# Kernel tuning notes

Hardware: AMD Instinct MI355X
Metric: run time of the kernel (lower is better)

The kernel has to match this reference:

```python
import jax, jax.numpy as jnp
import numpy as np
from jax import lax


def conv2d(x, w, b, pad):
    y = lax.conv_general_dilated(x, w, (1, 1), [(pad, pad), (pad, pad)],
                                 dimension_numbers=('NCHW', 'OIHW', 'NCHW'))
    return y + b[None, :, None, None]


def grid_sample_bilinear_border(img, grid):
    # img [B,C,H,W], grid [B,h,w,2] normalized to [-1,1] (x,y), align_corners=False
    B, C, H, W = img.shape
    gx, gy = grid[..., 0], grid[..., 1]
    ix = jnp.clip(((gx + 1.0) * W - 1.0) * 0.5, 0.0, W - 1.0)  # border padding = clamp coords
    iy = jnp.clip(((gy + 1.0) * H - 1.0) * 0.5, 0.0, H - 1.0)
    x0f, y0f = jnp.floor(ix), jnp.floor(iy)
    wx, wy = ix - x0f, iy - y0f                       # [B,h,w]
    x0 = jnp.clip(x0f.astype(jnp.int32), 0, W - 1)
    y0 = jnp.clip(y0f.astype(jnp.int32), 0, H - 1)
    x1 = jnp.clip(x0 + 1, 0, W - 1)
    y1 = jnp.clip(y0 + 1, 0, H - 1)
    gather = jax.vmap(lambda im, yi, xi: im[:, yi, xi])  # -> [B,C,h,w]
    v00 = gather(img, y0, x0)
    v01 = gather(img, y0, x1)
    v10 = gather(img, y1, x0)
    v11 = gather(img, y1, x1)
    wx, wy = wx[:, None], wy[:, None]                  # [B,1,h,w]
    return (v00 * (1 - wx) * (1 - wy) + v01 * wx * (1 - wy)
            + v10 * (1 - wx) * wy + v11 * wx * wy)


def setup_inputs():
    key = jax.random.key(0)
    ks = jax.random.split(key, 16)
    B, Ch, H, W = 8, 256, 64, 64
    Cl, h, w = 128, 128, 128
    Co, r = 128, 8
    s = 0.05
    return {
        'f_high': jax.random.normal(ks[0], (B, Ch, H, W), jnp.float32),
        'f_low': jax.random.normal(ks[1], (B, Cl, h, w), jnp.float32),
        'off_w1': jax.random.normal(ks[2], (64, Ch + Cl, 3, 3), jnp.float32) * s,
        'off_b1': jnp.zeros((64,), jnp.float32),
        'off_w2': jax.random.normal(ks[3], (2, 64, 3, 3), jnp.float32) * s,
        'off_b2': jnp.zeros((2,), jnp.float32),
        'proj_w': jax.random.normal(ks[4], (Co, Ch), jnp.float32) * s,
        'proj_b': jnp.zeros((Co,), jnp.float32),
        'ca_w1': jax.random.normal(ks[5], (Co // r, Co), jnp.float32) * s,
        'ca_b1': jnp.zeros((Co // r,), jnp.float32),
        'ca_w2': jax.random.normal(ks[6], (Co, Co // r), jnp.float32) * s,
        'ca_b2': jnp.zeros((Co,), jnp.float32),
        'sa_w': jax.random.normal(ks[7], (1, 2, 7, 7), jnp.float32) * s,
        'sa_b': jnp.zeros((1,), jnp.float32),
    }


def reference(f_high, f_low, off_w1, off_b1, off_w2, off_b2,
              proj_w, proj_b, ca_w1, ca_b1, ca_w2, ca_b2, sa_w, sa_b):
    B, Ch, H, W = f_high.shape
    _, Cl, h, w = f_low.shape
    # resize f_high to (h,w) (bilinear, half-pixel centers == align_corners=False)
    fh_r = jax.image.resize(f_high, (B, Ch, h, w), 'bilinear', antialias=False)
    cat = jnp.concatenate([fh_r, f_low], axis=1)       # [B,Ch+Cl,h,w]
    hid = jax.nn.relu(conv2d(cat, off_w1, off_b1, 1))
    offset = conv2d(hid, off_w2, off_b2, 1)            # [B,2,h,w]
    # base normalized grid (x,y) in [-1,1]
    ys = jnp.linspace(-1.0, 1.0, h, dtype=f_high.dtype)
    xs = jnp.linspace(-1.0, 1.0, w, dtype=f_high.dtype)
    gy, gx = jnp.meshgrid(ys, xs, indexing='ij')
    base = jnp.stack([gx, gy], axis=-1)[None]          # [1,h,w,2]
    scale = jnp.array([2.0 / w, 2.0 / h], dtype=f_high.dtype)
    grid = base + offset.transpose(0, 2, 3, 1) * scale  # [B,h,w,2]
    f_aligned = grid_sample_bilinear_border(f_high, grid)  # [B,Ch,h,w]
    # 1x1 proj Ch -> Co
    x = jnp.einsum('oc,bchw->bohw', proj_w, f_aligned) + proj_b[None, :, None, None]
    # multi-attention fusion: channel (SE) then spatial (CBAM-style)
    p = x.mean(axis=(2, 3))                            # [B,Co]
    a = jax.nn.sigmoid(jax.nn.relu(p @ ca_w1.T + ca_b1) @ ca_w2.T + ca_b2)
    xc = x * a[:, :, None, None]
    sm = jnp.concatenate([xc.mean(axis=1, keepdims=True),
                          xc.max(axis=1, keepdims=True)], axis=1)  # [B,2,h,w]
    sa = jax.nn.sigmoid(conv2d(sm, sa_w, sa_b, 3))
    return xc * sa
```

## Files before the change

kernel.cpp:

```cpp
#include <hip/hip_runtime.h>
#include <hip/hip_fp16.h>
#include <math.h>

typedef _Float16 f16;
typedef _Float16 f16x8 __attribute__((ext_vector_type(8)));
typedef _Float16 f16x2 __attribute__((ext_vector_type(2)));
typedef float f32x4 __attribute__((ext_vector_type(4)));

__device__ __forceinline__ void gll16(const void* g, void* l) {
  __builtin_amdgcn_global_load_lds((const __attribute__((address_space(1))) void*)g,
                                   (__attribute__((address_space(3))) void*)l, 16, 0, 0);
}

__global__ __launch_bounds__(256) void pack_conv_w(const float* __restrict__ w,
                                                   f16* __restrict__ out,
                                                   int CIN, int MFR, int COUT) {
  int idx = blockIdx.x * 256 + threadIdx.x;
  int KC = CIN / 32;
  int total = 9 * KC * MFR * 64 * 8;
  if (idx >= total) return;
  int j = idx & 7;
  int lane = (idx >> 3) & 63;
  int rest = idx >> 9;
  int mf = rest % MFR; rest /= MFR;
  int kc = rest % KC; int t = rest / KC;
  int oc = mf * 16 + (lane & 15);
  int c = kc * 32 + (lane >> 4) * 8 + j;
  int ky = t / 3, kx = t % 3;
  float v = (oc < COUT) ? w[((oc * CIN + c) * 3 + ky) * 3 + kx] : 0.f;
  out[idx] = (f16)v;
}

__global__ __launch_bounds__(256) void pack_proj_w(const float* __restrict__ w,
                                                   f16* __restrict__ out) {
  int idx = blockIdx.x * 256 + threadIdx.x;
  int j = idx & 7; int lane = (idx >> 3) & 63; int rest = idx >> 9;
  int mf = rest & 7; int kc = rest >> 3;
  int oc = mf * 16 + (lane & 15);
  int c = kc * 32 + (lane >> 4) * 8 + j;
  out[idx] = (f16)w[oc * 256 + c];
}

__global__ __launch_bounds__(256) void k_zero(f16* __restrict__ cat, f16* __restrict__ hid) {
  int idx = blockIdx.x * 256 + threadIdx.x;
  f16x8 z = {(f16)0, (f16)0, (f16)0, (f16)0, (f16)0, (f16)0, (f16)0, (f16)0};
  int p, b, c8;
  f16* dst; int C;
  if (idx < 198144) {
    c8 = idx % 48; int rest = idx / 48; p = rest % 516; b = rest / 516;
    dst = cat; C = 384;
  } else {
    int i2 = idx - 198144;
    c8 = i2 % 8; int rest = i2 / 8; p = rest % 516; b = rest / 516;
    dst = hid; C = 64;
  }
  int y, x;
  if (p < 130) { y = 0; x = p; }
  else if (p < 260) { y = 129; x = p - 130; }
  else if (p < 388) { y = p - 260 + 1; x = 0; }
  else { y = p - 388 + 1; x = 129; }
  *(f16x8*)&dst[(((size_t)b * 130 + y) * 130 + x) * C + c8 * 8] = z;
}

__global__ __launch_bounds__(256) void k_fhw(const float* __restrict__ fh,
                                             f16* __restrict__ fhw) {
  __shared__ float lds[128 * 17];
  int wg = blockIdx.x;
  int xt = wg & 3; int ch2 = (wg >> 2) & 1; int y = (wg >> 3) & 63; int b = wg >> 9;
  int x0 = xt * 16;
  int tid = threadIdx.x;
  for (int i = 0; i < 8; ++i) {
    int u = i * 256 + tid;
    int c = u >> 4, xi = u & 15;
    lds[c * 17 + xi] = fh[(((size_t)b * 256 + ch2 * 128 + c) * 64 + y) * 64 + x0 + xi];
  }
  __syncthreads();
  {
    int x = tid >> 4, cl = tid & 15;
    f16x8 v;
    #pragma unroll
    for (int j = 0; j < 8; ++j) v[j] = (f16)lds[(cl * 8 + j) * 17 + x];
    int coct = ch2 * 16 + cl;
    *(f16x8*)&fhw[(((size_t)b * 64 + y) * 64 + x0 + x) * 256 + coct * 8] = v;
  }
}

__global__ __launch_bounds__(256) void k_catA(const f16* __restrict__ fhw,
                                              f16* __restrict__ cat) {
  int wg = blockIdx.x;
  int Y = wg & 127, b = wg >> 7;
  float iy = fminf(fmaxf(Y * 0.5f - 0.25f, 0.f), 63.f);
  int y0 = (int)iy; float wy = iy - y0; int y1 = min(y0 + 1, 63);
  int tid = threadIdx.x;
  for (int i = 0; i < 16; ++i) {
    int u = i * 256 + tid; int X = u >> 5, coct = u & 31;
    float ix = fminf(fmaxf(X * 0.5f - 0.25f, 0.f), 63.f);
    int x0 = (int)ix; float wx = ix - x0; int x1 = min(x0 + 1, 63);
    f16x8 v00 = *(const f16x8*)&fhw[(((size_t)b * 64 + y0) * 64 + x0) * 256 + coct * 8];
    f16x8 v01 = *(const f16x8*)&fhw[(((size_t)b * 64 + y0) * 64 + x1) * 256 + coct * 8];
    f16x8 v10 = *(const f16x8*)&fhw[(((size_t)b * 64 + y1) * 64 + x0) * 256 + coct * 8];
    f16x8 v11 = *(const f16x8*)&fhw[(((size_t)b * 64 + y1) * 64 + x1) * 256 + coct * 8];
    f16x8 r;
    #pragma unroll
    for (int j = 0; j < 8; ++j) {
      float t0 = (1.f - wx) * (float)v00[j] + wx * (float)v01[j];
      float t1 = (1.f - wx) * (float)v10[j] + wx * (float)v11[j];
      r[j] = (f16)((1.f - wy) * t0 + wy * t1);
    }
    *(f16x8*)&cat[(((size_t)b * 130 + 1 + Y) * 130 + 1 + X) * 384 + coct * 8] = r;
  }
}

__global__ __launch_bounds__(256) void k_catB(const float* __restrict__ fl,
                                              f16* __restrict__ cat) {
  __shared__ float lds[128 * 17];
  int wg = blockIdx.x;
  int xt = wg & 7; int Y = (wg >> 3) & 127; int b = wg >> 10;
  int x0 = xt * 16; int tid = threadIdx.x;
  for (int i = 0; i < 8; ++i) {
    int u = i * 256 + tid; int c = u >> 4, xi = u & 15;
    lds[c * 17 + xi] = fl[(((size_t)b * 128 + c) * 128 + Y) * 128 + x0 + xi];
  }
  __syncthreads();
  {
    int x = tid >> 4, coct = tid & 15;
    f16x8 v;
    #pragma unroll
    for (int j = 0; j < 8; ++j) v[j] = (f16)lds[(coct * 8 + j) * 17 + x];
    *(f16x8*)&cat[(((size_t)b * 130 + 1 + Y) * 130 + 1 + x0 + x) * 384 + 256 + coct * 8] = v;
  }
}

template<int CIN, int MFR, int COUT, bool RELU, int OPAD, int NR, bool FORCE1>
__global__ __launch_bounds__(256, FORCE1 ? 1 : 2) void k_conv3(const f16* __restrict__ in,
                                                               const f16* __restrict__ apack,
                                                               const float* __restrict__ bias,
                                                               f16* __restrict__ out) {
  constexpr int KC = CIN / 32;
  constexpr int TROWS = 4 * NR;
  constexpr int TY = 128 / TROWS;
  constexpr int NSLOT = (TROWS + 2) * 18 * 4;
  constexpr int NPAD = (NSLOT + 255) & ~255;
  constexpr int ROUNDS = NPAD / 256;
  constexpr int PATCH = NPAD * 16;
  constexpr int EPI = TROWS * 16 * COUT * 2;
  constexpr int LDS_SZ = (2 * PATCH > EPI ? 2 * PATCH : EPI) + (FORCE1 ? 1024 : 0);
  __shared__ __align__(16) char ldsb[LDS_SZ];
  int wg = blockIdx.x;
  int b = wg & 7; int t = wg >> 3;
  int ty = t % TY, tx = t / TY;
  int y0 = ty * TROWS, x0 = tx * 16;
  int tid = threadIdx.x, lane = tid & 63, w = tid >> 6;
  int lx = lane & 15, hi = lane >> 4;
  int wN = w * NR;

  int ro[ROUNDS];
  #pragma unroll
  for (int j = 0; j < ROUNDS; ++j) {
    int s = j * 256 + w * 64 + lane;
    if (s > NSLOT - 1) s = NSLOT - 1;
    int p = s >> 2, coct = s & 3;
    int py = p / 18, px = p % 18;
    int cocts = coct ^ ((px >> 1) & 3);
    ro[j] = ((y0 + py) * 130 + (x0 + px)) * CIN + cocts * 8;
  }
  const f16* inb = in + (size_t)b * 130 * 130 * CIN;

  f32x4 acc[MFR][NR];
  #pragma unroll
  for (int m = 0; m < MFR; ++m)
    #pragma unroll
    for (int n = 0; n < NR; ++n) acc[m][n] = (f32x4){0.f, 0.f, 0.f, 0.f};

  auto stage = [&](int kc, int buf) {
    #pragma unroll
    for (int j = 0; j < ROUNDS; ++j)
      gll16(inb + ro[j] + kc * 32, ldsb + buf * PATCH + (j * 256 + w * 64) * 16);
  };

  stage(0, 0);
  __syncthreads();
  for (int kc = 0; kc < KC; ++kc) {
    if (kc + 1 < KC) stage(kc + 1, (kc + 1) & 1);
    const char* cb = ldsb + (kc & 1) * PATCH;
    __builtin_amdgcn_s_setprio(1);
    #pragma unroll
    for (int kx = 0; kx < 3; ++kx) {
      int px = lx + kx;
      int sw = (px >> 1) & 3;
      f16x8 bf[NR + 2];
      #pragma unroll
      for (int s = 0; s < NR + 2; ++s) {
        int slot = ((wN + s) * 18 + px) * 4 + (hi ^ sw);
        bf[s] = *(const f16x8*)(cb + slot * 16);
      }
      #pragma unroll
      for (int ky = 0; ky < 3; ++ky) {
        f16x8 af[MFR];
        #pragma unroll
        for (int m = 0; m < MFR; ++m)
          af[m] = *(const f16x8*)&apack[(size_t)((((ky * 3 + kx) * KC + kc) * MFR + m) * 64 + lane) * 8];
        #pragma unroll
        for (int n = 0; n < NR; ++n)
          #pragma unroll
          for (int m = 0; m < MFR; ++m)
            acc[m][n] = __builtin_amdgcn_mfma_f32_16x16x32_f16(af[m], bf[n + ky], acc[m][n], 0, 0, 0);
      }
    }
    __builtin_amdgcn_s_setprio(0);
    __syncthreads();
  }

  constexpr int S = 128 + 2 * OPAD;
  #pragma unroll
  for (int m = 0; m < MFR; ++m)
    #pragma unroll
    for (int n = 0; n < NR; ++n) {
      int pos = (wN + n) * 16 + lx;
      #pragma unroll
      for (int rp = 0; rp < 2; ++rp) {
        int ch = m * 16 + hi * 4 + rp * 2;
        if (ch < COUT) {
          float v0 = acc[m][n][rp * 2 + 0] + bias[ch];
          float v1 = acc[m][n][rp * 2 + 1] + bias[ch + 1];
          if (RELU) { v0 = fmaxf(v0, 0.f); v1 = fmaxf(v1, 0.f); }
          f16x2 pk; pk[0] = (f16)v0; pk[1] = (f16)v1;
          int addr = ((pos * COUT + ch) * 2) ^ ((pos & 7) << 4);
          *(f16x2*)(ldsb + addr) = pk;
        }
      }
    }
  __syncthreads();
  if constexpr (COUT % 8 == 0) {
    for (int u = tid; u < TROWS * 16 * COUT / 8; u += 256) {
      int pos = u / (COUT / 8); int cp = u % (COUT / 8);
      int addr = ((pos * COUT + cp * 8) * 2) ^ ((pos & 7) << 4);
      f16x8 v = *(const f16x8*)(ldsb + addr);
      int y = y0 + (pos >> 4) + OPAD, x = x0 + (pos & 15) + OPAD;
      *(f16x8*)&out[(((size_t)b * S + y) * S + x) * COUT + cp * 8] = v;
    }
  } else {
    for (int u = tid; u < TROWS * 16 * COUT / 2; u += 256) {
      int pos = u / (COUT / 2); int cp = u % (COUT / 2);
      int addr = ((pos * COUT + cp * 2) * 2) ^ ((pos & 7) << 4);
      f16x2 v = *(const f16x2*)(ldsb + addr);
      int y = y0 + (pos >> 4) + OPAD, x = x0 + (pos & 15) + OPAD;
      *(f16x2*)&out[(((size_t)b * S + y) * S + x) * COUT + cp * 2] = v;
    }
  }
}

__global__ __launch_bounds__(256) void k_gp(const f16* __restrict__ fhw,
                                            const f16* __restrict__ off,
                                            const f16* __restrict__ ppack,
                                            const float* __restrict__ pbias,
                                            f16* __restrict__ x,
                                            float* __restrict__ psum) {
  __shared__ f16 bt[64 * 256];
  __shared__ float4 samp[64];
  char* ldsb = (char*)bt;
  int wg = blockIdx.x;
  int b = wg & 7, tile = wg >> 3;
  int pbase = tile * 64;
  int tid = threadIdx.x, lane = tid & 63, w = tid >> 6;
  if (tid < 64) {
    int pos = pbase + tid;
    int yy = pos >> 7, xx = pos & 127;
    float o0 = (float)off[((size_t)b * 16384 + pos) * 2 + 0];
    float o1 = (float)off[((size_t)b * 16384 + pos) * 2 + 1];
    float gx = -1.f + xx * (2.f / 127.f) + o0 * (1.f / 64.f);
    float gy = -1.f + yy * (2.f / 127.f) + o1 * (1.f / 64.f);
    float ix = fminf(fmaxf((gx + 1.f) * 32.f - 0.5f, 0.f), 63.f);
    float iy = fminf(fmaxf((gy + 1.f) * 32.f - 0.5f, 0.f), 63.f);
    float x0f = floorf(ix), y0f = floorf(iy);
    samp[tid] = make_float4(x0f, y0f, ix - x0f, iy - y0f);
  }
  __syncthreads();
  for (int i = 0; i < 8; ++i) {
    int u = i * 256 + tid; int p = u >> 5, coct = u & 31;
    float4 s = samp[p];
    int x0i = (int)s.x, y0i = (int)s.y;
    int x1i = min(x0i + 1, 63), y1i = min(y0i + 1, 63);
    float wx = s.z, wy = s.w;
    const f16* bb = fhw + (size_t)b * 4096 * 256 + coct * 8;
    f16x8 v00 = *(const f16x8*)&bb[(y0i * 64 + x0i) * 256];
    f16x8 v01 = *(const f16x8*)&bb[(y0i * 64 + x1i) * 256];
    f16x8 v10 = *(const f16x8*)&bb[(y1i * 64 + x0i) * 256];
    f16x8 v11 = *(const f16x8*)&bb[(y1i * 64 + x1i) * 256];
    f16x8 r;
    #pragma unroll
    for (int j = 0; j < 8; ++j) {
      float t0 = (1.f - wx) * (float)v00[j] + wx * (float)v01[j];
      float t1 = (1.f - wx) * (float)v10[j] + wx * (float)v11[j];
      r[j] = (f16)((1.f - wy) * t0 + wy * t1);
    }
    int addr = (p * 512 + coct * 16) ^ ((p & 7) << 4);
    *(f16x8*)(ldsb + addr) = r;
  }
  __syncthreads();
  f32x4 acc[2][4];
  #pragma unroll
  for (int m = 0; m < 2; ++m)
    #pragma unroll
    for (int n = 0; n < 4; ++n) acc[m][n] = (f32x4){0.f, 0.f, 0.f, 0.f};
  #pragma unroll
  for (int kc = 0; kc < 8; ++kc) {
    f16x8 af[2];
    #pragma unroll
    for (int m = 0; m < 2; ++m)
      af[m] = *(const f16x8*)&ppack[(size_t)((kc * 8 + w * 2 + m) * 64 + lane) * 8];
    #pragma unroll
    for (int n = 0; n < 4; ++n) {
      int p = n * 16 + (lane & 15);
      int addr = (p * 512 + kc * 64 + ((lane >> 4) * 16)) ^ ((p & 7) << 4);
      f16x8 bf = *(const f16x8*)(ldsb + addr);
      #pragma unroll
      for (int m = 0; m < 2; ++m)
        acc[m][n] = __builtin_amdgcn_mfma_f32_16x16x32_f16(af[m], bf, acc[m][n], 0, 0, 0);
    }
  }
  __syncthreads();
  #pragma unroll
  for (int m = 0; m < 2; ++m)
    #pragma unroll
    for (int n = 0; n < 4; ++n) {
      int p = n * 16 + (lane & 15);
      #pragma unroll
      for (int r = 0; r < 4; ++r) {
        int ch = w * 32 + m * 16 + (lane >> 4) * 4 + r;
        int addr = ((p * 128 + ch) * 4) ^ ((p & 7) << 4);
        *(float*)(ldsb + addr) = acc[m][n][r];
      }
    }
  __syncthreads();
  float part0 = 0.f, part1 = 0.f;
  int cp = tid & 63, wv = tid >> 6;
  int c0 = cp * 2;
  float b0 = pbias[c0], b1 = pbias[c0 + 1];
  #pragma unroll
  for (int i = 0; i < 16; ++i) {
    int p = i * 4 + wv;
    float v0 = *(const float*)(ldsb + (((p * 128 + c0) * 4) ^ ((p & 7) << 4)));
    float v1 = *(const float*)(ldsb + (((p * 128 + c0 + 1) * 4) ^ ((p & 7) << 4)));
    v0 += b0; v1 += b1;
    f16x2 pk; pk[0] = (f16)v0; pk[1] = (f16)v1;
    *(f16x2*)&x[((size_t)b * 16384 + pbase + p) * 128 + c0] = pk;
    part0 += v0; part1 += v1;
  }
  __syncthreads();
  float* rl = (float*)ldsb;
  rl[wv * 128 + c0] = part0; rl[wv * 128 + c0 + 1] = part1;
  __syncthreads();
  if (tid < 128)
    psum[(size_t)wg * 128 + tid] = rl[tid] + rl[128 + tid] + rl[256 + tid] + rl[384 + tid];
}

__global__ __launch_bounds__(128) void k_ca(const float* __restrict__ psum,
                                            const float* __restrict__ w1, const float* __restrict__ b1,
                                            const float* __restrict__ w2, const float* __restrict__ b2,
                                            float* __restrict__ a) {
  __shared__ float pl[128];
  __shared__ float hl[16];
  int b = blockIdx.x; int tid = threadIdx.x;
  float s = 0.f;
  for (int t = 0; t < 256; ++t) s += psum[(size_t)(t * 8 + b) * 128 + tid];
  pl[tid] = s * (1.f / 16384.f);
  __syncthreads();
  if (tid < 16) {
    float h = b1[tid];
    for (int c = 0; c < 128; ++c) h += pl[c] * w1[tid * 128 + c];
    hl[tid] = fmaxf(h, 0.f);
  }
  __syncthreads();
  float z = b2[tid];
  #pragma unroll
  for (int o2 = 0; o2 < 16; ++o2) z += hl[o2] * w2[tid * 16 + o2];
  a[b * 128 + tid] = 1.f / (1.f + expf(-z));
}

__global__ __launch_bounds__(256) void k_sm(const f16* __restrict__ x,
                                            const float* __restrict__ a,
                                            float* __restrict__ meanp, float* __restrict__ maxp) {
  __shared__ float al[128];
  int wg = blockIdx.x;
  int pbase = wg * 128;
  int b = pbase >> 14;
  int tid = threadIdx.x;
  if (tid < 128) al[tid] = a[b * 128 + tid];
  __syncthreads();
  #pragma unroll
  for (int i = 0; i < 8; ++i) {
    int u = i * 256 + tid;
    int p = u >> 4, q = u & 15;
    f16x8 v = *(const f16x8*)&x[((size_t)pbase + p) * 128 + q * 8];
    float sm = 0.f, mx = -1e30f;
    #pragma unroll
    for (int j = 0; j < 8; ++j) {
      float xc = (float)v[j] * al[q * 8 + j];
      sm += xc; mx = fmaxf(mx, xc);
    }
    #pragma unroll
    for (int d = 1; d < 16; d <<= 1) {
      sm += __shfl_xor(sm, d);
      mx = fmaxf(mx, __shfl_xor(mx, d));
    }
    if ((tid & 15) == 0) {
      meanp[pbase + p] = sm * (1.f / 128.f);
      maxp[pbase + p] = mx;
    }
  }
}

__global__ __launch_bounds__(256) void k_sa(const float* __restrict__ meanp,
                                            const float* __restrict__ maxp,
                                            const float* __restrict__ sw, const float* __restrict__ sb,
                                            float* __restrict__ sap) {
  __shared__ float lds[2][22][22];
  __shared__ float wl[98];
  int wg = blockIdx.x;
  int tx = wg & 7, ty = (wg >> 3) & 7, b = wg >> 6;
  int y0 = ty * 16, x0 = tx * 16;
  int tid = threadIdx.x;
  if (tid < 98) wl[tid] = sw[tid];
  for (int u = tid; u < 2 * 22 * 22; u += 256) {
    int ch = u / 484; int p = u % 484; int py = p / 22, px = p % 22;
    int gy = y0 + py - 3, gx = x0 + px - 3;
    float v = 0.f;
    if (gy >= 0 && gy < 128 && gx >= 0 && gx < 128)
      v = ch ? maxp[(size_t)b * 16384 + gy * 128 + gx] : meanp[(size_t)b * 16384 + gy * 128 + gx];
    lds[ch][py][px] = v;
  }
  __syncthreads();
  int py = tid >> 4, px = tid & 15;
  float accv = sb[0];
  #pragma unroll
  for (int ch = 0; ch < 2; ++ch)
    for (int ky = 0; ky < 7; ++ky)
      #pragma unroll
      for (int kx = 0; kx < 7; ++kx)
        accv += lds[ch][py + ky][px + kx] * wl[ch * 49 + ky * 7 + kx];
  sap[(size_t)b * 16384 + (y0 + py) * 128 + x0 + px] = 1.f / (1.f + expf(-accv));
}

__global__ __launch_bounds__(256) void k_out(const f16* __restrict__ x,
                                             const float* __restrict__ a,
                                             const float* __restrict__ sap,
                                             float* __restrict__ out) {
  __shared__ float lds[32 * 129];
  __shared__ float al[128];
  __shared__ float sl[32];
  int wg = blockIdx.x;
  int pbase = wg * 32; int b = pbase >> 14;
  int tid = threadIdx.x;
  if (tid < 128) al[tid] = a[b * 128 + tid];
  if (tid < 32) sl[tid] = sap[pbase + tid];
  __syncthreads();
  #pragma unroll
  for (int i = 0; i < 2; ++i) {
    int u = i * 256 + tid;
    int p = u >> 4, q = u & 15;
    f16x8 v = *(const f16x8*)&x[((size_t)pbase + p) * 128 + q * 8];
    #pragma unroll
    for (int j = 0; j < 8; ++j) lds[p * 129 + q * 8 + j] = (float)v[j];
  }
  __syncthreads();
  #pragma unroll
  for (int i = 0; i < 16; ++i) {
    int u = i * 256 + tid; int c = u >> 5, p = u & 31;
    float v = lds[p * 129 + c] * al[c] * sl[p];
    out[((size_t)(b * 128 + c)) * 16384 + (pbase & 16383) + p] = v;
  }
}

extern "C" void kernel_launch(void* const* d_in, const int* in_sizes, int n_in,
                              void* d_out, int out_size, void* d_ws, size_t ws_size,
                              hipStream_t stream) {
  const float* f_high = (const float*)d_in[0];
  const float* f_low  = (const float*)d_in[1];
  const float* off_w1 = (const float*)d_in[2];
  const float* off_b1 = (const float*)d_in[3];
  const float* off_w2 = (const float*)d_in[4];
  const float* off_b2 = (const float*)d_in[5];
  const float* proj_w = (const float*)d_in[6];
  const float* proj_b = (const float*)d_in[7];
  const float* ca_w1  = (const float*)d_in[8];
  const float* ca_b1  = (const float*)d_in[9];
  const float* ca_w2  = (const float*)d_in[10];
  const float* ca_b2  = (const float*)d_in[11];
  const float* sa_w   = (const float*)d_in[12];
  const float* sa_b   = (const float*)d_in[13];
  float* out = (float*)d_out;

  char* ws = (char*)d_ws; size_t o = 0;
  auto alloc = [&](size_t b) { char* p = ws + o; o += (b + 255) & ~(size_t)255; return p; };
  f16*   fhw  = (f16*)alloc(8ull * 4096 * 256 * 2);
  f16*   cat  = (f16*)alloc(8ull * 130 * 130 * 384 * 2);
  f16*   hid  = (f16*)alloc(8ull * 130 * 130 * 64 * 2);
  f16*   offb = (f16*)alloc(8ull * 16384 * 2 * 2);
  f16*   ap1  = (f16*)alloc(221184ull * 2);
  f16*   ap2  = (f16*)alloc(9216ull * 2);
  f16*   pp   = (f16*)alloc(32768ull * 2);
  f16*   xbuf = (f16*)alloc(8ull * 16384 * 128 * 2);
  float* ps   = (float*)alloc(2048ull * 128 * 4);
  float* av   = (float*)alloc(8ull * 128 * 4);
  float* mp   = (float*)alloc(131072ull * 4);
  float* xp   = (float*)alloc(131072ull * 4);
  float* sp   = (float*)alloc(131072ull * 4);

  pack_conv_w<<<864, 256, 0, stream>>>(off_w1, ap1, 384, 4, 64);
  pack_conv_w<<<36, 256, 0, stream>>>(off_w2, ap2, 64, 1, 2);
  pack_proj_w<<<128, 256, 0, stream>>>(proj_w, pp);
  k_zero<<<903, 256, 0, stream>>>(cat, hid);
  k_fhw<<<4096, 256, 0, stream>>>(f_high, fhw);
  k_catA<<<1024, 256, 0, stream>>>(fhw, cat);
  k_catB<<<8192, 256, 0, stream>>>(f_low, cat);
  k_conv3<384, 4, 64, true, 1, 8, true><<<256, 256, 0, stream>>>(cat, ap1, off_b1, hid);
  k_conv3<64, 1, 2, false, 0, 4, false><<<512, 256, 0, stream>>>(hid, ap2, off_b2, offb);
  k_gp<<<2048, 256, 0, stream>>>(fhw, offb, pp, proj_b, xbuf, ps);
  k_ca<<<8, 128, 0, stream>>>(ps, ca_w1, ca_b1, ca_w2, ca_b2, av);
  k_sm<<<1024, 256, 0, stream>>>(xbuf, av, mp, xp);
  k_sa<<<512, 256, 0, stream>>>(mp, xp, sa_w, sa_b, sp);
  k_out<<<4096, 256, 0, stream>>>(xbuf, av, sp, out);
}
```

Before: 358.2 us.

## Merge prep kernels, add dedicated conv1 kernel with split output channels, widen k_ca

Five small preparation kernels (weight packing, border zeroing, f_high transpose) become one launch, and the two concat kernels become another, reducing launch count and inter-kernel gaps. The first 3x3 conv moves to a specialized kernel with 512 workgroups, where each wave covers half the output channels over 8 rows. The weight packing order changes to kc-major to match. The channel-attention kernel now uses 256 threads to split its reduction. The cost is more branchy merged kernels and different register and LDS pressure in the new conv.

```diff
diff --git a/kernel.cpp b/kernel.cpp
--- a/kernel.cpp
+++ b/kernel.cpp
@@ -12,10 +12,8 @@
                                    (__attribute__((address_space(3))) void*)l, 16, 0, 0);
 }
 
-__global__ __launch_bounds__(256) void pack_conv_w(const float* __restrict__ w,
-                                                   f16* __restrict__ out,
-                                                   int CIN, int MFR, int COUT) {
-  int idx = blockIdx.x * 256 + threadIdx.x;
+__device__ __forceinline__ void pack_conv_body(int idx, const float* __restrict__ w,
+                                               f16* __restrict__ out, int CIN, int MFR, int COUT) {
   int KC = CIN / 32;
   int total = 9 * KC * MFR * 64 * 8;
   if (idx >= total) return;
@@ -23,7 +21,7 @@
   int lane = (idx >> 3) & 63;
   int rest = idx >> 9;
   int mf = rest % MFR; rest /= MFR;
-  int kc = rest % KC; int t = rest / KC;
+  int t = rest % 9; int kc = rest / 9;
   int oc = mf * 16 + (lane & 15);
   int c = kc * 32 + (lane >> 4) * 8 + j;
   int ky = t / 3, kx = t % 3;
@@ -31,51 +29,66 @@
   out[idx] = (f16)v;
 }
 
-__global__ __launch_bounds__(256) void pack_proj_w(const float* __restrict__ w,
-                                                   f16* __restrict__ out) {
-  int idx = blockIdx.x * 256 + threadIdx.x;
-  int j = idx & 7; int lane = (idx >> 3) & 63; int rest = idx >> 9;
-  int mf = rest & 7; int kc = rest >> 3;
-  int oc = mf * 16 + (lane & 15);
-  int c = kc * 32 + (lane >> 4) * 8 + j;
-  out[idx] = (f16)w[oc * 256 + c];
-}
-
-__global__ __launch_bounds__(256) void k_zero(f16* __restrict__ cat, f16* __restrict__ hid) {
-  int idx = blockIdx.x * 256 + threadIdx.x;
-  f16x8 z = {(f16)0, (f16)0, (f16)0, (f16)0, (f16)0, (f16)0, (f16)0, (f16)0};
-  int p, b, c8;
-  f16* dst; int C;
-  if (idx < 198144) {
-    c8 = idx % 48; int rest = idx / 48; p = rest % 516; b = rest / 516;
-    dst = cat; C = 384;
-  } else {
-    int i2 = idx - 198144;
-    c8 = i2 % 8; int rest = i2 / 8; p = rest % 516; b = rest / 516;
-    dst = hid; C = 64;
-  }
-  int y, x;
-  if (p < 130) { y = 0; x = p; }
-  else if (p < 260) { y = 129; x = p - 130; }
-  else if (p < 388) { y = p - 260 + 1; x = 0; }
-  else { y = p - 388 + 1; x = 129; }
-  *(f16x8*)&dst[(((size_t)b * 130 + y) * 130 + x) * C + c8 * 8] = z;
-}
-
-__global__ __launch_bounds__(256) void k_fhw(const float* __restrict__ fh,
-                                             f16* __restrict__ fhw) {
-  __shared__ float lds[128 * 17];
-  int wg = blockIdx.x;
-  int xt = wg & 3; int ch2 = (wg >> 2) & 1; int y = (wg >> 3) & 63; int b = wg >> 9;
-  int x0 = xt * 16;
+__global__ __launch_bounds__(256) void k_prep(const float* __restrict__ off_w1, f16* __restrict__ ap1,
+                                              const float* __restrict__ off_w2, f16* __restrict__ ap2,
+                                              const float* __restrict__ proj_w, f16* __restrict__ pp,
+                                              f16* __restrict__ cat, f16* __restrict__ hid,
+                                              const float* __restrict__ fh, f16* __restrict__ fhw) {
+  int blk = blockIdx.x;
   int tid = threadIdx.x;
-  for (int i = 0; i < 8; ++i) {
-    int u = i * 256 + tid;
-    int c = u >> 4, xi = u & 15;
-    lds[c * 17 + xi] = fh[(((size_t)b * 256 + ch2 * 128 + c) * 64 + y) * 64 + x0 + xi];
-  }
-  __syncthreads();
+  if (blk < 864) {
+    pack_conv_body(blk * 256 + tid, off_w1, ap1, 384, 4, 64);
+    return;
+  }
+  blk -= 864;
+  if (blk < 36) {
+    pack_conv_body(blk * 256 + tid, off_w2, ap2, 64, 1, 2);
+    return;
+  }
+  blk -= 36;
+  if (blk < 128) {
+    int idx = blk * 256 + tid;
+    int j = idx & 7; int lane = (idx >> 3) & 63; int rest = idx >> 9;
+    int mf = rest & 7; int kc = rest >> 3;
+    int oc = mf * 16 + (lane & 15);
+    int c = kc * 32 + (lane >> 4) * 8 + j;
+    pp[idx] = (f16)proj_w[oc * 256 + c];
+    return;
+  }
+  blk -= 128;
+  if (blk < 903) {
+    int idx = blk * 256 + tid;
+    if (idx >= 231168) return;
+    f16x8 z = {(f16)0, (f16)0, (f16)0, (f16)0, (f16)0, (f16)0, (f16)0, (f16)0};
+    int p, b, c8;
+    f16* dst; int C;
+    if (idx < 198144) {
+      c8 = idx % 48; int rest = idx / 48; p = rest % 516; b = rest / 516;
+      dst = cat; C = 384;
+    } else {
+      int i2 = idx - 198144;
+      c8 = i2 % 8; int rest = i2 / 8; p = rest % 516; b = rest / 516;
+      dst = hid; C = 64;
+    }
+    int y, x;
+    if (p < 130) { y = 0; x = p; }
+    else if (p < 260) { y = 129; x = p - 130; }
+    else if (p < 388) { y = p - 260 + 1; x = 0; }
+    else { y = p - 388 + 1; x = 129; }
+    *(f16x8*)&dst[(((size_t)b * 130 + y) * 130 + x) * C + c8 * 8] = z;
+    return;
+  }
+  blk -= 903;
   {
+    __shared__ float lds[128 * 17];
+    int xt = blk & 3; int ch2 = (blk >> 2) & 1; int y = (blk >> 3) & 63; int b = blk >> 9;
+    int x0 = xt * 16;
+    for (int i = 0; i < 8; ++i) {
+      int u = i * 256 + tid;
+      int c = u >> 4, xi = u & 15;
+      lds[c * 17 + xi] = fh[(((size_t)b * 256 + ch2 * 128 + c) * 64 + y) * 64 + x0 + xi];
+    }
+    __syncthreads();
     int x = tid >> 4, cl = tid & 15;
     f16x8 v;
     #pragma unroll
@@ -85,44 +98,44 @@
   }
 }
 
-__global__ __launch_bounds__(256) void k_catA(const f16* __restrict__ fhw,
-                                              f16* __restrict__ cat) {
-  int wg = blockIdx.x;
-  int Y = wg & 127, b = wg >> 7;
-  float iy = fminf(fmaxf(Y * 0.5f - 0.25f, 0.f), 63.f);
-  int y0 = (int)iy; float wy = iy - y0; int y1 = min(y0 + 1, 63);
+__global__ __launch_bounds__(256) void k_cat(const f16* __restrict__ fhw,
+                                             const float* __restrict__ fl,
+                                             f16* __restrict__ cat) {
+  int blk = blockIdx.x;
   int tid = threadIdx.x;
-  for (int i = 0; i < 16; ++i) {
-    int u = i * 256 + tid; int X = u >> 5, coct = u & 31;
-    float ix = fminf(fmaxf(X * 0.5f - 0.25f, 0.f), 63.f);
-    int x0 = (int)ix; float wx = ix - x0; int x1 = min(x0 + 1, 63);
-    f16x8 v00 = *(const f16x8*)&fhw[(((size_t)b * 64 + y0) * 64 + x0) * 256 + coct * 8];
-    f16x8 v01 = *(const f16x8*)&fhw[(((size_t)b * 64 + y0) * 64 + x1) * 256 + coct * 8];
-    f16x8 v10 = *(const f16x8*)&fhw[(((size_t)b * 64 + y1) * 64 + x0) * 256 + coct * 8];
-    f16x8 v11 = *(const f16x8*)&fhw[(((size_t)b * 64 + y1) * 64 + x1) * 256 + coct * 8];
-    f16x8 r;
-    #pragma unroll
-    for (int j = 0; j < 8; ++j) {
-      float t0 = (1.f - wx) * (float)v00[j] + wx * (float)v01[j];
-      float t1 = (1.f - wx) * (float)v10[j] + wx * (float)v11[j];
-      r[j] = (f16)((1.f - wy) * t0 + wy * t1);
-    }
-    *(f16x8*)&cat[(((size_t)b * 130 + 1 + Y) * 130 + 1 + X) * 384 + coct * 8] = r;
-  }
-}
-
-__global__ __launch_bounds__(256) void k_catB(const float* __restrict__ fl,
-                                              f16* __restrict__ cat) {
-  __shared__ float lds[128 * 17];
-  int wg = blockIdx.x;
-  int xt = wg & 7; int Y = (wg >> 3) & 127; int b = wg >> 10;
-  int x0 = xt * 16; int tid = threadIdx.x;
-  for (int i = 0; i < 8; ++i) {
-    int u = i * 256 + tid; int c = u >> 4, xi = u & 15;
-    lds[c * 17 + xi] = fl[(((size_t)b * 128 + c) * 128 + Y) * 128 + x0 + xi];
-  }
-  __syncthreads();
+  if (blk < 1024) {
+    int Y = blk & 127, b = blk >> 7;
+    float iy = fminf(fmaxf(Y * 0.5f - 0.25f, 0.f), 63.f);
+    int y0 = (int)iy; float wy = iy - y0; int y1 = min(y0 + 1, 63);
+    for (int i = 0; i < 16; ++i) {
+      int u = i * 256 + tid; int X = u >> 5, coct = u & 31;
+      float ix = fminf(fmaxf(X * 0.5f - 0.25f, 0.f), 63.f);
+      int x0 = (int)ix; float wx = ix - x0; int x1 = min(x0 + 1, 63);
+      f16x8 v00 = *(const f16x8*)&fhw[(((size_t)b * 64 + y0) * 64 + x0) * 256 + coct * 8];
+      f16x8 v01 = *(const f16x8*)&fhw[(((size_t)b * 64 + y0) * 64 + x1) * 256 + coct * 8];
+      f16x8 v10 = *(const f16x8*)&fhw[(((size_t)b * 64 + y1) * 64 + x0) * 256 + coct * 8];
+      f16x8 v11 = *(const f16x8*)&fhw[(((size_t)b * 64 + y1) * 64 + x1) * 256 + coct * 8];
+      f16x8 r;
+      #pragma unroll
+      for (int j = 0; j < 8; ++j) {
+        float t0 = (1.f - wx) * (float)v00[j] + wx * (float)v01[j];
+        float t1 = (1.f - wx) * (float)v10[j] + wx * (float)v11[j];
+        r[j] = (f16)((1.f - wy) * t0 + wy * t1);
+      }
+      *(f16x8*)&cat[(((size_t)b * 130 + 1 + Y) * 130 + 1 + X) * 384 + coct * 8] = r;
+    }
+    return;
+  }
+  blk -= 1024;
   {
+    __shared__ float lds[128 * 17];
+    int xt = blk & 7; int Y = (blk >> 3) & 127; int b = blk >> 10;
+    int x0 = xt * 16;
+    for (int i = 0; i < 8; ++i) {
+      int u = i * 256 + tid; int c = u >> 4, xi = u & 15;
+      lds[c * 17 + xi] = fl[(((size_t)b * 128 + c) * 128 + Y) * 128 + x0 + xi];
+    }
+    __syncthreads();
     int x = tid >> 4, coct = tid & 15;
     f16x8 v;
     #pragma unroll
@@ -131,11 +144,111 @@
   }
 }
 
-template<int CIN, int MFR, int COUT, bool RELU, int OPAD, int NR, bool FORCE1>
-__global__ __launch_bounds__(256, FORCE1 ? 1 : 2) void k_conv3(const f16* __restrict__ in,
-                                                               const f16* __restrict__ apack,
-                                                               const float* __restrict__ bias,
-                                                               f16* __restrict__ out) {
+__global__ __launch_bounds__(256) void k_conv1(const f16* __restrict__ in,
+                                               const f16* __restrict__ apack,
+                                               const float* __restrict__ bias,
+                                               f16* __restrict__ out) {
+  constexpr int KC = 12;
+  constexpr int NSLOT = 1296;
+  constexpr int PATCH = 1536 * 16;
+  __shared__ __align__(16) char ldsb[2 * PATCH];
+  int wg = blockIdx.x;
+  int b = wg & 7; int t = wg >> 3;
+  int ty = t & 7, tx = t >> 3;
+  int y0 = ty * 16, x0 = tx * 16;
+  int tid = threadIdx.x, lane = tid & 63, w = tid >> 6;
+  int lx = lane & 15, hi = lane >> 4;
+  int mfh = w & 1, rbase = (w >> 1) * 8;
+
+  int ro[6];
+  #pragma unroll
+  for (int j = 0; j < 6; ++j) {
+    int s = j * 256 + tid;
+    if (s > NSLOT - 1) s = NSLOT - 1;
+    int p = s >> 2, coct = s & 3;
+    int py = p / 18, px = p % 18;
+    int cocts = coct ^ ((px >> 1) & 3);
+    ro[j] = ((y0 + py) * 130 + (x0 + px)) * 384 + cocts * 8;
+  }
+  const f16* inb = in + (size_t)b * 130 * 130 * 384;
+
+  f32x4 acc[2][8];
+  #pragma unroll
+  for (int m = 0; m < 2; ++m)
+    #pragma unroll
+    for (int n = 0; n < 8; ++n) acc[m][n] = (f32x4){0.f, 0.f, 0.f, 0.f};
+
+  auto stage = [&](int kc, int buf) {
+    #pragma unroll
+    for (int j = 0; j < 6; ++j)
+      gll16(inb + ro[j] + kc * 32, ldsb + buf * PATCH + (j * 256 + tid) * 16);
+  };
+
+  stage(0, 0);
+  __syncthreads();
+  for (int kc = 0; kc < KC; ++kc) {
+    if (kc + 1 < KC) stage(kc + 1, (kc + 1) & 1);
+    const char* cb = ldsb + (kc & 1) * PATCH;
+    __builtin_amdgcn_s_setprio(1);
+    #pragma unroll
+    for (int kx = 0; kx < 3; ++kx) {
+      int px = lx + kx;
+      int sw = (px >> 1) & 3;
+      f16x8 bf[10];
+      #pragma unroll
+      for (int s = 0; s < 10; ++s) {
+        int slot = ((rbase + s) * 18 + px) * 4 + (hi ^ sw);
+        bf[s] = *(const f16x8*)(cb + slot * 16);
+      }
+      #pragma unroll
+      for (int ky = 0; ky < 3; ++ky) {
+        f16x8 af[2];
+        #pragma unroll
+        for (int m = 0; m < 2; ++m)
+          af[m] = *(const f16x8*)&apack[(size_t)(((kc * 9 + ky * 3 + kx) * 4 + mfh * 2 + m) * 64 + lane) * 8];
+        #pragma unroll
+        for (int n = 0; n < 8; ++n)
+          #pragma unroll
+          for (int m = 0; m < 2; ++m)
+            acc[m][n] = __builtin_amdgcn_mfma_f32_16x16x32_f16(af[m], bf[n + ky], acc[m][n], 0, 0, 0);
+      }
+    }
+    __builtin_amdgcn_s_setprio(0);
+    __syncthreads();
+  }
+
+  #pragma unroll
+  for (int m = 0; m < 2; ++m)
+    #pragma unroll
+    for (int n = 0; n < 8; ++n) {
+      int pos = (rbase + n) * 16 + lx;
+      #pragma unroll
+      for (int rp = 0; rp < 2; ++rp) {
+        int ch = mfh * 32 + m * 16 + hi * 4 + rp * 2;
+        float v0 = fmaxf(acc[m][n][rp * 2 + 0] + bias[ch], 0.f);
+        float v1 = fmaxf(acc[m][n][rp * 2 + 1] + bias[ch + 1], 0.f);
+        f16x2 pk; pk[0] = (f16)v0; pk[1] = (f16)v1;
+        int addr = ((pos * 64 + ch) * 2) ^ ((pos & 7) << 4);
+        *(f16x2*)(ldsb + addr) = pk;
+      }
+    }
+  __syncthreads();
+  #pragma unroll
+  for (int i = 0; i < 8; ++i) {
+    int u = i * 256 + tid;
+    int pos = u >> 3, cp = u & 7;
+    int addr = ((pos * 64 + cp * 8) * 2) ^ ((pos & 7) << 4);
+    f16x8 v = *(const f16x8*)(ldsb + addr);
+    int y = y0 + (pos >> 4) + 1, x = x0 + (pos & 15) + 1;
+    *(f16x8*)&out[(((size_t)b * 130 + y) * 130 + x) * 64 + cp * 8] = v;
+  }
+}
+
+template<int CIN, int MFR, int COUT, bool RELU, int OPAD, int NR>
+__global__ __launch_bounds__(256, 2) void k_conv3(const f16* __restrict__ in,
+                                                  const f16* __restrict__ apack,
+                                                  const float* __restrict__ bias,
+                                                  f16* __restrict__ out) {
   constexpr int KC = CIN / 32;
   constexpr int TROWS = 4 * NR;
   constexpr int TY = 128 / TROWS;
@@ -144,7 +257,7 @@
   constexpr int ROUNDS = NPAD / 256;
   constexpr int PATCH = NPAD * 16;
   constexpr int EPI = TROWS * 16 * COUT * 2;
-  constexpr int LDS_SZ = (2 * PATCH > EPI ? 2 * PATCH : EPI) + (FORCE1 ? 1024 : 0);
+  constexpr int LDS_SZ = (2 * PATCH > EPI ? 2 * PATCH : EPI);
   __shared__ __align__(16) char ldsb[LDS_SZ];
   int wg = blockIdx.x;
   int b = wg & 7; int t = wg >> 3;
@@ -157,7 +270,7 @@
   int ro[ROUNDS];
   #pragma unroll
   for (int j = 0; j < ROUNDS; ++j) {
-    int s = j * 256 + w * 64 + lane;
+    int s = j * 256 + tid;
     if (s > NSLOT - 1) s = NSLOT - 1;
     int p = s >> 2, coct = s & 3;
     int py = p / 18, px = p % 18;
@@ -175,7 +288,7 @@
   auto stage = [&](int kc, int buf) {
     #pragma unroll
     for (int j = 0; j < ROUNDS; ++j)
-      gll16(inb + ro[j] + kc * 32, ldsb + buf * PATCH + (j * 256 + w * 64) * 16);
+      gll16(inb + ro[j] + kc * 32, ldsb + buf * PATCH + (j * 256 + tid) * 16);
   };
 
   stage(0, 0);
@@ -199,7 +312,7 @@
         f16x8 af[MFR];
         #pragma unroll
         for (int m = 0; m < MFR; ++m)
-          af[m] = *(const f16x8*)&apack[(size_t)((((ky * 3 + kx) * KC + kc) * MFR + m) * 64 + lane) * 8];
+          af[m] = *(const f16x8*)&apack[(size_t)(((kc * 9 + ky * 3 + kx) * MFR + m) * 64 + lane) * 8];
         #pragma unroll
         for (int n = 0; n < NR; ++n)
           #pragma unroll
@@ -231,22 +344,12 @@
       }
     }
   __syncthreads();
-  if constexpr (COUT % 8 == 0) {
-    for (int u = tid; u < TROWS * 16 * COUT / 8; u += 256) {
-      int pos = u / (COUT / 8); int cp = u % (COUT / 8);
-      int addr = ((pos * COUT + cp * 8) * 2) ^ ((pos & 7) << 4);
-      f16x8 v = *(const f16x8*)(ldsb + addr);
-      int y = y0 + (pos >> 4) + OPAD, x = x0 + (pos & 15) + OPAD;
-      *(f16x8*)&out[(((size_t)b * S + y) * S + x) * COUT + cp * 8] = v;
-    }
-  } else {
-    for (int u = tid; u < TROWS * 16 * COUT / 2; u += 256) {
-      int pos = u / (COUT / 2); int cp = u % (COUT / 2);
-      int addr = ((pos * COUT + cp * 2) * 2) ^ ((pos & 7) << 4);
-      f16x2 v = *(const f16x2*)(ldsb + addr);
-      int y = y0 + (pos >> 4) + OPAD, x = x0 + (pos & 15) + OPAD;
-      *(f16x2*)&out[(((size_t)b * S + y) * S + x) * COUT + cp * 2] = v;
-    }
+  for (int u = tid; u < TROWS * 16 * COUT / 2; u += 256) {
+    int pos = u / (COUT / 2); int cp = u % (COUT / 2);
+    int addr = ((pos * COUT + cp * 2) * 2) ^ ((pos & 7) << 4);
+    f16x2 v = *(const f16x2*)(ldsb + addr);
+    int y = y0 + (pos >> 4) + OPAD, x = x0 + (pos & 15) + OPAD;
+    *(f16x2*)&out[(((size_t)b * S + y) * S + x) * COUT + cp * 2] = v;
   }
 }
 
@@ -355,27 +458,34 @@
     psum[(size_t)wg * 128 + tid] = rl[tid] + rl[128 + tid] + rl[256 + tid] + rl[384 + tid];
 }
 
-__global__ __launch_bounds__(128) void k_ca(const float* __restrict__ psum,
+__global__ __launch_bounds__(256) void k_ca(const float* __restrict__ psum,
                                             const float* __restrict__ w1, const float* __restrict__ b1,
                                             const float* __restrict__ w2, const float* __restrict__ b2,
                                             float* __restrict__ a) {
+  __shared__ float red[256];
   __shared__ float pl[128];
   __shared__ float hl[16];
   int b = blockIdx.x; int tid = threadIdx.x;
+  int half = tid >> 7, c = tid & 127;
   float s = 0.f;
-  for (int t = 0; t < 256; ++t) s += psum[(size_t)(t * 8 + b) * 128 + tid];
-  pl[tid] = s * (1.f / 16384.f);
+  for (int i = 0; i < 128; ++i)
+    s += psum[(size_t)((i * 2 + half) * 8 + b) * 128 + c];
+  red[tid] = s;
+  __syncthreads();
+  if (tid < 128) pl[tid] = (red[tid] + red[tid + 128]) * (1.f / 16384.f);
   __syncthreads();
   if (tid < 16) {
     float h = b1[tid];
-    for (int c = 0; c < 128; ++c) h += pl[c] * w1[tid * 128 + c];
+    for (int cc = 0; cc < 128; ++cc) h += pl[cc] * w1[tid * 128 + cc];
     hl[tid] = fmaxf(h, 0.f);
   }
   __syncthreads();
-  float z = b2[tid];
-  #pragma unroll
-  for (int o2 = 0; o2 < 16; ++o2) z += hl[o2] * w2[tid * 16 + o2];
-  a[b * 128 + tid] = 1.f / (1.f + expf(-z));
+  if (tid < 128) {
+    float z = b2[tid];
+    #pragma unroll
+    for (int o2 = 0; o2 < 16; ++o2) z += hl[o2] * w2[tid * 16 + o2];
+    a[b * 128 + tid] = 1.f / (1.f + expf(-z));
+  }
 }
 
 __global__ __launch_bounds__(256) void k_sm(const f16* __restrict__ x,
@@ -507,17 +617,13 @@
   float* xp   = (float*)alloc(131072ull * 4);
   float* sp   = (float*)alloc(131072ull * 4);
 
-  pack_conv_w<<<864, 256, 0, stream>>>(off_w1, ap1, 384, 4, 64);
-  pack_conv_w<<<36, 256, 0, stream>>>(off_w2, ap2, 64, 1, 2);
-  pack_proj_w<<<128, 256, 0, stream>>>(proj_w, pp);
-  k_zero<<<903, 256, 0, stream>>>(cat, hid);
-  k_fhw<<<4096, 256, 0, stream>>>(f_high, fhw);
-  k_catA<<<1024, 256, 0, stream>>>(fhw, cat);
-  k_catB<<<8192, 256, 0, stream>>>(f_low, cat);
-  k_conv3<384, 4, 64, true, 1, 8, true><<<256, 256, 0, stream>>>(cat, ap1, off_b1, hid);
-  k_conv3<64, 1, 2, false, 0, 4, false><<<512, 256, 0, stream>>>(hid, ap2, off_b2, offb);
+  k_prep<<<864 + 36 + 128 + 903 + 4096, 256, 0, stream>>>(off_w1, ap1, off_w2, ap2,
+                                                          proj_w, pp, cat, hid, f_high, fhw);
+  k_cat<<<1024 + 8192, 256, 0, stream>>>(fhw, f_low, cat);
+  k_conv1<<<512, 256, 0, stream>>>(cat, ap1, off_b1, hid);
+  k_conv3<64, 1, 2, false, 0, 4><<<512, 256, 0, stream>>>(hid, ap2, off_b2, offb);
   k_gp<<<2048, 256, 0, stream>>>(fhw, offb, pp, proj_b, xbuf, ps);
-  k_ca<<<8, 128, 0, stream>>>(ps, ca_w1, ca_b1, ca_w2, ca_b2, av);
+  k_ca<<<8, 256, 0, stream>>>(ps, ca_w1, ca_b1, ca_w2, ca_b2, av);
   k_sm<<<1024, 256, 0, stream>>>(xbuf, av, mp, xp);
   k_sa<<<512, 256, 0, stream>>>(mp, xp, sa_w, sa_b, sp);
   k_out<<<4096, 256, 0, stream>>>(xbuf, av, sp, out);
```

Result: faster. 327.7 us (-8.5%).
